# Kernel tuning notes

Hardware: AMD Instinct MI355X
Metric: run time of the kernel (lower is better)

## Reference

```python
import jax, jax.numpy as jnp
import numpy as np

D_MODEL = 1024
NUM_HEADS = 16
D_K = D_MODEL // NUM_HEADS


def setup_inputs() -> dict:
    key = jax.random.key(0)
    ks = jax.random.split(key, 9)
    s = 1.0 / np.sqrt(D_MODEL)
    return {
        "z": jax.random.normal(ks[0], (4, 2048, D_MODEL), dtype=jnp.float32),
        "Wq": jax.random.uniform(ks[1], (D_MODEL, D_MODEL), jnp.float32, -s, s),
        "bq": jax.random.uniform(ks[2], (D_MODEL,), jnp.float32, -s, s),
        "Wk": jax.random.uniform(ks[3], (D_MODEL, D_MODEL), jnp.float32, -s, s),
        "bk": jax.random.uniform(ks[4], (D_MODEL,), jnp.float32, -s, s),
        "Wv": jax.random.uniform(ks[5], (D_MODEL, D_MODEL), jnp.float32, -s, s),
        "bv": jax.random.uniform(ks[6], (D_MODEL,), jnp.float32, -s, s),
        "Wo": jax.random.uniform(ks[7], (D_MODEL, D_MODEL), jnp.float32, -s, s),
        "bo": jax.random.uniform(ks[8], (D_MODEL,), jnp.float32, -s, s),
    }


def reference(z, Wq, bq, Wk, bk, Wv, bv, Wo, bo):
    B, S, _ = z.shape
    # project and split heads: [B, H, S, d_k]
    def proj(W, b):
        return (z @ W.T + b).reshape(B, S, NUM_HEADS, D_K).transpose(0, 2, 1, 3)
    Q, K, V = proj(Wq, bq), proj(Wk, bk), proj(Wv, bv)
    scale = 1.0 / np.sqrt(D_K)
    scores = jnp.einsum('bhqd,bhkd->bhqk', Q, K) * scale
    probs = jax.nn.softmax(scores, axis=-1)
    ctx = jnp.einsum('bhqk,bhkd->bhqd', probs, V)
    ctx = ctx.transpose(0, 2, 1, 3).reshape(B, S, D_MODEL)
    return ctx @ Wo.T + bo
```

## Files before the change

### kernel.cpp

```cpp
#include <hip/hip_runtime.h>
#include <stdint.h>

#define D_MODEL 1024
#define NHEAD 16
#define DKH 64
#define BATCH 4
#define SEQ 2048
#define M_ROWS (BATCH*SEQ)
#define NBH (BATCH*NHEAD)

typedef float f32x4 __attribute__((ext_vector_type(4)));
typedef float f32x16 __attribute__((ext_vector_type(16)));
typedef __bf16 bf16x8 __attribute__((ext_vector_type(8)));
typedef __bf16 bf16x4v __attribute__((ext_vector_type(4)));
typedef short short4v __attribute__((ext_vector_type(4)));
typedef unsigned short ushort4v __attribute__((ext_vector_type(4)));
typedef unsigned short ushort8v __attribute__((ext_vector_type(8)));
typedef unsigned int uint2v __attribute__((ext_vector_type(2)));

__device__ __forceinline__ unsigned short f2bf(float x) {
    __bf16 b = (__bf16)x;
    return __builtin_bit_cast(unsigned short, b);
}

#define GLL(gsrc, ldst) \
    __builtin_amdgcn_global_load_lds((const __attribute__((address_space(1))) void*)(gsrc), \
                                     (__attribute__((address_space(3))) void*)(ldst), 16, 0, 0)


__device__ __forceinline__ void cvt8store(const float* __restrict__ src,
                                          unsigned short* __restrict__ dst) {
    float4 v0 = *(const float4*)(src);
    float4 v1 = *(const float4*)(src + 4);
    ushort8v o;
    o[0] = f2bf(v0.x); o[1] = f2bf(v0.y); o[2] = f2bf(v0.z); o[3] = f2bf(v0.w);
    o[4] = f2bf(v1.x); o[5] = f2bf(v1.y); o[6] = f2bf(v1.z); o[7] = f2bf(v1.w);
    *(ushort8v*)dst = o;
}

__global__ __launch_bounds__(256) void k_convert(
    const float* __restrict__ z,  const float* __restrict__ wq,
    const float* __restrict__ wk, const float* __restrict__ wv,
    const float* __restrict__ wo,
    const float* __restrict__ bq, const float* __restrict__ bk,
    const float* __restrict__ bv,
    unsigned short* __restrict__ zf, unsigned short* __restrict__ wqkvf,
    unsigned short* __restrict__ wobf, float* __restrict__ biasf)
{
    int i = blockIdx.x * 256 + threadIdx.x;
    if (i < 1048576) {
        int lane = i & 63, rest = i >> 6;
        int kk = rest & 1, mfrag = (rest >> 1) & 7, half = (rest >> 4) & 1;
        int kt = (rest >> 5) & 15, mtile = rest >> 9;
        int row = mtile * 256 + half * 128 + mfrag * 16 + (lane & 15);
        int k = kt * 64 + kk * 32 + (lane >> 4) * 8;
        cvt8store(z + (size_t)row * 1024 + k, zf + (size_t)i * 8);
    }
    int i2 = i - 1048576;
    if (i2 >= 0 && i2 < 393216) {
        int lane = i2 & 63, rest = i2 >> 6;
        int kk = rest & 1, nfrag = (rest >> 1) & 7;
        int kt = (rest >> 4) & 15, ntile = rest >> 8;
        int n = ntile * 128 + nfrag * 16 + (lane & 15);
        int k = kt * 64 + kk * 32 + (lane >> 4) * 8;
        const float* W = (n < 1024) ? wq : ((n < 2048) ? wk : wv);
        cvt8store(W + (size_t)(n & 1023) * 1024 + k, wqkvf + (size_t)i2 * 8);
    }
    int i3 = i2 - 393216;
    if (i3 >= 0 && i3 < 131072) {
        int lane = i3 & 63, rest = i3 >> 6;
        int kk = rest & 1, nfrag = (rest >> 1) & 7;
        int kt = (rest >> 4) & 15, ntile = rest >> 8;
        int n = ntile * 128 + nfrag * 16 + (lane & 15);
        int k = kt * 64 + kk * 32 + (lane >> 4) * 8;
        cvt8store(wo + (size_t)n * 1024 + k, wobf + (size_t)i3 * 8);
    }
    if (i < 1024) {
        biasf[i]        = bq[i];
        biasf[1024 + i] = bk[i];
        biasf[2048 + i] = bv[i];
    }
}

__device__ __forceinline__ void g_stage(const unsigned short* __restrict__ as_,
                                        const unsigned short* __restrict__ bs_,
                                        unsigned short* la, unsigned short* lb,
                                        int wid, int lane)
{
#pragma unroll
    for (int g = 0; g < 4; ++g)
        GLL(as_ + (wid + 8 * g) * 512 + lane * 8, la + (wid + 8 * g) * 512);
#pragma unroll
    for (int g = 0; g < 2; ++g)
        GLL(bs_ + (wid + 8 * g) * 512 + lane * 8, lb + (wid + 8 * g) * 512);
}

#define GEMM_KLOOP(Abase, Bbase)                                                      \
    g_stage(Abase, Bbase, &ldsA[0][0], &ldsB[0][0], wid, lane);                       \
    g_stage(Abase + 16384, Bbase + 8192, &ldsA[1][0], &ldsB[1][0], wid, lane);        \
    asm volatile("s_waitcnt vmcnt(6)" ::: "memory");                                  \
    __builtin_amdgcn_s_barrier();                                                     \
    for (int t = 0; t < 16; ++t) {                                                    \
        int buf = t % 3;                                                              \
        if (t + 2 < 16)                                                               \
            g_stage(Abase + (size_t)(t + 2) * 16384, Bbase + (size_t)(t + 2) * 8192,  \
                    &ldsA[(t + 2) % 3][0], &ldsB[(t + 2) % 3][0], wid, lane);         \
        const unsigned short* A = &ldsA[buf][0];                                      \
        const unsigned short* B = &ldsB[buf][0];                                      \
        bf16x8 b00 = *(const bf16x8*)(B + ((wn * 2 + 0) * 2 + 0) * 512 + lane * 8);   \
        bf16x8 b01 = *(const bf16x8*)(B + ((wn * 2 + 0) * 2 + 1) * 512 + lane * 8);   \
        bf16x8 b10 = *(const bf16x8*)(B + ((wn * 2 + 1) * 2 + 0) * 512 + lane * 8);   \
        bf16x8 b11 = *(const bf16x8*)(B + ((wn * 2 + 1) * 2 + 1) * 512 + lane * 8);   \
        _Pragma("unroll")                                                             \
        for (int ii = 0; ii < 8; ++ii) {                                              \
            bf16x8 a0 = *(const bf16x8*)(A + ((wm * 8 + ii) * 2 + 0) * 512 + lane * 8); \
            bf16x8 a1 = *(const bf16x8*)(A + ((wm * 8 + ii) * 2 + 1) * 512 + lane * 8); \
            acc[ii][0] = __builtin_amdgcn_mfma_f32_16x16x32_bf16(a0, b00, acc[ii][0], 0, 0, 0); \
            acc[ii][0] = __builtin_amdgcn_mfma_f32_16x16x32_bf16(a1, b01, acc[ii][0], 0, 0, 0); \
            acc[ii][1] = __builtin_amdgcn_mfma_f32_16x16x32_bf16(a0, b10, acc[ii][1], 0, 0, 0); \
            acc[ii][1] = __builtin_amdgcn_mfma_f32_16x16x32_bf16(a1, b11, acc[ii][1], 0, 0, 0); \
        }                                                                             \
        if (t < 14)       { asm volatile("s_waitcnt vmcnt(6)" ::: "memory"); }        \
        else if (t == 14) { asm volatile("s_waitcnt vmcnt(0)" ::: "memory"); }        \
        if (t < 15) { __builtin_amdgcn_sched_barrier(0); __builtin_amdgcn_s_barrier(); } \
    }

__global__ __launch_bounds__(512) void k_gemm_qkv(
    const unsigned short* __restrict__ Af,
    const unsigned short* __restrict__ Bf,
    const float* __restrict__ biasf,
    unsigned short* __restrict__ qb, unsigned short* __restrict__ kfrag,
    unsigned short* __restrict__ vfrag)
{
    __shared__ unsigned short ldsA[3][16384];
    __shared__ unsigned short ldsB[3][8192];

    int bid = blockIdx.x;
    int wg = (bid & 7) * 96 + (bid >> 3);
    int tn = wg % 24, tm = wg / 24;
    int tid = threadIdx.x, wid = tid >> 6, lane = tid & 63;
    int wm = wid >> 2, wn = wid & 3;

    const unsigned short* Abase = Af + (size_t)tm * 16 * 16384;
    const unsigned short* Bbase = Bf + (size_t)tn * 16 * 8192;

    f32x4 acc[8][2] = {};
    GEMM_KLOOP(Abase, Bbase)

    const float QSC = 0.18033688011112042f;
    int t3 = tn >> 3;
#pragma unroll
    for (int j = 0; j < 2; ++j) {
        int col = tn * 128 + wn * 32 + j * 16 + (lane & 15);
        float bias = biasf[col];
        int d = col & 1023, h = d >> 6, dk = d & 63;
#pragma unroll
        for (int i = 0; i < 8; ++i) {
#pragma unroll
            for (int r = 0; r < 4; ++r) {
                int row = tm * 256 + wm * 128 + i * 16 + (lane >> 4) * 4 + r;
                float v = acc[i][j][r] + bias;
                if (t3 == 0) v *= QSC;
                unsigned short bv16 = f2bf(v);
                int b_ = row >> 11, s_ = row & 2047;
                int bh = b_ * NHEAD + h;
                if (t3 == 0) {
                    qb[((size_t)bh * SEQ + s_) * DKH + dk] = bv16;
                } else if (t3 == 1) {
                    int kvblk = s_ >> 6, r64 = s_ & 63;
                    int t32 = r64 >> 5, l5 = r64 & 31;
                    int ds = dk >> 4, hi2 = (dk >> 3) & 1, e = dk & 7;
                    kfrag[((size_t)(bh * 32 + kvblk)) * 4096 +
                          (t32 * 4 + ds) * 512 + (hi2 * 32 + l5) * 8 + e] = bv16;
                } else {
                    int kvblk = s_ >> 6, kv64 = s_ & 63;
                    int ks = kv64 >> 3, hi2 = (kv64 >> 2) & 1, e = kv64 & 3;
                    int vt = dk >> 5, l5 = dk & 31;
                    vfrag[((size_t)(bh * 32 + kvblk)) * 4096 +
                          (vt * 8 + ks) * 256 + (hi2 * 32 + l5) * 4 + e] = bv16;
                }
            }
        }
    }
}

#define ATTN_STEP(LDSK, LDSV, WPREV, WCUR, DO_PV)                                   \
    {                                                                               \
        f32x16 st0 = {}, st1 = {};                                                  \
        __builtin_amdgcn_s_setprio(1);                                              \
        _Pragma("unroll")                                                           \
        for (int ds = 0; ds < 4; ++ds) {                                            \
            bf16x8 kf0 = *(const bf16x8*)(&(LDSK)[(ds) * 512 + lane * 8]);          \
            bf16x8 kf1 = *(const bf16x8*)(&(LDSK)[(4 + ds) * 512 + lane * 8]);      \
            st0 = __builtin_amdgcn_mfma_f32_32x32x16_bf16(kf0, aq[ds], st0, 0, 0, 0); \
            st1 = __builtin_amdgcn_mfma_f32_32x32x16_bf16(kf1, aq[ds], st1, 0, 0, 0); \
            if (DO_PV) {                                                            \
                short4v vf0 = *(const short4v*)(&(LDSV)[(2 * ds) * 256 + lane * 4]);        \
                short4v vf1 = *(const short4v*)(&(LDSV)[(8 + 2 * ds) * 256 + lane * 4]);    \
                oa0 = __builtin_amdgcn_mfma_f32_32x32x8bf16_1k(vf0, WPREV[2 * ds], oa0, 0, 0, 0); \
                oa1 = __builtin_amdgcn_mfma_f32_32x32x8bf16_1k(vf1, WPREV[2 * ds], oa1, 0, 0, 0); \
                short4v vf2 = *(const short4v*)(&(LDSV)[(2 * ds + 1) * 256 + lane * 4]);    \
                short4v vf3 = *(const short4v*)(&(LDSV)[(8 + 2 * ds + 1) * 256 + lane * 4]);\
                oa0 = __builtin_amdgcn_mfma_f32_32x32x8bf16_1k(vf2, WPREV[2 * ds + 1], oa0, 0, 0, 0); \
                oa1 = __builtin_amdgcn_mfma_f32_32x32x8bf16_1k(vf3, WPREV[2 * ds + 1], oa1, 0, 0, 0); \
            }                                                                       \
        }                                                                           \
        __builtin_amdgcn_s_setprio(0);                                              \
        _Pragma("unroll")                                                           \
        for (int ks = 0; ks < 4; ++ks) {                                            \
            {                                                                       \
                float p0 = __builtin_amdgcn_exp2f(st0[4 * ks + 0]);                 \
                float p1 = __builtin_amdgcn_exp2f(st0[4 * ks + 1]);                 \
                float p2 = __builtin_amdgcn_exp2f(st0[4 * ks + 2]);                 \
                float p3 = __builtin_amdgcn_exp2f(st0[4 * ks + 3]);                 \
                lsum += (p0 + p1) + (p2 + p3);                                      \
                bf16x4v pb;                                                         \
                pb[0] = (__bf16)p0; pb[1] = (__bf16)p1; pb[2] = (__bf16)p2; pb[3] = (__bf16)p3; \
                WCUR[ks] = __builtin_bit_cast(short4v, pb);                         \
            }                                                                       \
            {                                                                       \
                float p0 = __builtin_amdgcn_exp2f(st1[4 * ks + 0]);                 \
                float p1 = __builtin_amdgcn_exp2f(st1[4 * ks + 1]);                 \
                float p2 = __builtin_amdgcn_exp2f(st1[4 * ks + 2]);                 \
                float p3 = __builtin_amdgcn_exp2f(st1[4 * ks + 3]);                 \
                lsum += (p0 + p1) + (p2 + p3);                                      \
                bf16x4v pb;                                                         \
                pb[0] = (__bf16)p0; pb[1] = (__bf16)p1; pb[2] = (__bf16)p2; pb[3] = (__bf16)p3; \
                WCUR[4 + ks] = __builtin_bit_cast(short4v, pb);                     \
            }                                                                       \
        }                                                                           \
    }

#define DRAIN_BARRIER()                                         \
    asm volatile("s_waitcnt vmcnt(0)" ::: "memory");            \
    __builtin_amdgcn_sched_barrier(0);                          \
    __builtin_amdgcn_s_barrier();

__global__ __launch_bounds__(512) void k_attn(
    const unsigned short* __restrict__ qg,
    const unsigned short* __restrict__ kb,
    const unsigned short* __restrict__ vtb,
    unsigned short* __restrict__ ctxf)
{
    __shared__ unsigned short lds_k[2][4096];
    __shared__ unsigned short lds_v[2][4096];

    int bid = blockIdx.x;
    int x = bid & 7, li = bid >> 3;
    int bh = x * 8 + (li >> 3);
    int qt = li & 7;

    int tid = threadIdx.x, wid = tid >> 6, lane = tid & 63;
    int lq = lane & 31, hi = lane >> 5;

    bf16x8 aq[4];
    {
        const unsigned short* qp = qg + ((size_t)bh * SEQ + qt * 256 + wid * 32 + lq) * DKH + hi * 8;
#pragma unroll
        for (int d = 0; d < 4; ++d) aq[d] = *(const bf16x8*)(qp + d * 16);
    }

    float lsum = 0.f;
    f32x16 oa0 = {};
    f32x16 oa1 = {};
    short4v wA[8], wB[8];

    const unsigned short* kbase = kb  + (size_t)bh * 32 * 4096;
    const unsigned short* vbase = vtb + (size_t)bh * 32 * 4096;
    int so = wid * 512 + lane * 8;
    unsigned short* ldk0 = &lds_k[0][wid * 512];
    unsigned short* ldk1 = &lds_k[1][wid * 512];
    unsigned short* ldv0 = &lds_v[0][wid * 512];
    unsigned short* ldv1 = &lds_v[1][wid * 512];

    GLL(kbase + so, ldk0);
    DRAIN_BARRIER();

    GLL(kbase + 4096 + so, ldk1);
    GLL(vbase + so, ldv0);
    ATTN_STEP(lds_k[0], lds_v[0], wB, wA, false);
    DRAIN_BARRIER();

    for (int t = 1; t < 31; t += 2) {
        GLL(kbase + (size_t)(t + 1) * 4096 + so, ldk0);
        GLL(vbase + (size_t)t * 4096 + so, ldv1);
        ATTN_STEP(lds_k[1], lds_v[0], wA, wB, true);
        DRAIN_BARRIER();
        if (t + 2 < 32) GLL(kbase + (size_t)(t + 2) * 4096 + so, ldk1);
        GLL(vbase + (size_t)(t + 1) * 4096 + so, ldv0);
        ATTN_STEP(lds_k[0], lds_v[1], wB, wA, true);
        DRAIN_BARRIER();
    }

    GLL(vbase + (size_t)31 * 4096 + so, ldv1);
    ATTN_STEP(lds_k[1], lds_v[0], wA, wB, true);
    DRAIN_BARRIER();

    __builtin_amdgcn_s_setprio(1);
#pragma unroll
    for (int ks = 0; ks < 8; ++ks) {
        short4v vf0 = *(const short4v*)(&lds_v[1][(ks) * 256 + lane * 4]);
        short4v vf1 = *(const short4v*)(&lds_v[1][(8 + ks) * 256 + lane * 4]);
        oa0 = __builtin_amdgcn_mfma_f32_32x32x8bf16_1k(vf0, wB[ks], oa0, 0, 0, 0);
        oa1 = __builtin_amdgcn_mfma_f32_32x32x8bf16_1k(vf1, wB[ks], oa1, 0, 0, 0);
    }
    __builtin_amdgcn_s_setprio(0);

    int b_ = bh >> 4, h = bh & 15;
    lsum += __shfl_xor(lsum, 32);
    float inv = 1.0f / lsum;
    int s_ = qt * 256 + wid * 32 + lq;
    int row = b_ * 2048 + s_;
    int mtile = row >> 8, half = (row >> 7) & 1, mfrag = (row >> 4) & 7, lrow = row & 15;
    unsigned short* cb = ctxf + (size_t)((mtile * 16 + h) * 2 + half) * 8192
                              + mfrag * 1024 + lrow * 8 + 4 * hi;
#pragma unroll
    for (int m = 0; m < 4; ++m) {
        ushort4v s0, s1;
        s0[0] = f2bf(oa0[4 * m + 0] * inv); s0[1] = f2bf(oa0[4 * m + 1] * inv);
        s0[2] = f2bf(oa0[4 * m + 2] * inv); s0[3] = f2bf(oa0[4 * m + 3] * inv);
        *(ushort4v*)(cb + m * 128) = s0;
        s1[0] = f2bf(oa1[4 * m + 0] * inv); s1[1] = f2bf(oa1[4 * m + 1] * inv);
        s1[2] = f2bf(oa1[4 * m + 2] * inv); s1[3] = f2bf(oa1[4 * m + 3] * inv);
        *(ushort4v*)(cb + 512 + m * 128) = s1;
    }
}

__global__ __launch_bounds__(512) void k_gemm_out(
    const unsigned short* __restrict__ Af,
    const unsigned short* __restrict__ Bf,
    const float* __restrict__ bo,
    float* __restrict__ out)
{
    __shared__ unsigned short ldsA[3][16384];
    __shared__ unsigned short ldsB[3][8192];

    int bid = blockIdx.x;
    int wg = (bid & 7) * 32 + (bid >> 3);
    int tn = wg % 8, tm = wg / 8;
    int tid = threadIdx.x, wid = tid >> 6, lane = tid & 63;
    int wm = wid >> 2, wn = wid & 3;

    const unsigned short* Abase = Af + (size_t)tm * 16 * 16384;
    const unsigned short* Bbase = Bf + (size_t)tn * 16 * 8192;

    f32x4 acc[8][2] = {};
    GEMM_KLOOP(Abase, Bbase)

#pragma unroll
    for (int j = 0; j < 2; ++j) {
        int col = tn * 128 + wn * 32 + j * 16 + (lane & 15);
        float bias = bo[col];
#pragma unroll
        for (int i = 0; i < 8; ++i) {
#pragma unroll
            for (int r = 0; r < 4; ++r) {
                int row = tm * 256 + wm * 128 + i * 16 + (lane >> 4) * 4 + r;
                out[(size_t)row * 1024 + col] = acc[i][j][r] + bias;
            }
        }
    }
}

extern "C" void kernel_launch(void* const* d_in, const int* in_sizes, int n_in,
                              void* d_out, int out_size, void* d_ws, size_t ws_size,
                              hipStream_t stream)
{
    const float* z  = (const float*)d_in[0];
    const float* Wq = (const float*)d_in[1];
    const float* bq = (const float*)d_in[2];
    const float* Wk = (const float*)d_in[3];
    const float* bk = (const float*)d_in[4];
    const float* Wv = (const float*)d_in[5];
    const float* bv = (const float*)d_in[6];
    const float* Wo = (const float*)d_in[7];
    const float* bo = (const float*)d_in[8];
    float* out = (float*)d_out;

    char* ws = (char*)d_ws;
    unsigned short* zf    = (unsigned short*)(ws);
    unsigned short* ctxf  = (unsigned short*)(ws);
    unsigned short* wqkvf = (unsigned short*)(ws + (16ull << 20));
    unsigned short* wobf  = (unsigned short*)(ws + (22ull << 20));
    float*          biasf = (float*)(ws + (24ull << 20));
    unsigned short* qb    = (unsigned short*)(ws + (25ull << 20));
    unsigned short* kfrag = (unsigned short*)(ws + (41ull << 20));
    unsigned short* vfrag = (unsigned short*)(ws + (57ull << 20));

    k_convert<<<8192, 256, 0, stream>>>(z, Wq, Wk, Wv, Wo, bq, bk, bv, zf, wqkvf, wobf, biasf);
    k_gemm_qkv<<<768, 512, 0, stream>>>(zf, wqkvf, biasf, qb, kfrag, vfrag);
    k_attn<<<NBH * 8, 512, 0, stream>>>(qb, kfrag, vfrag, ctxf);
    k_gemm_out<<<256, 512, 0, stream>>>(ctxf, wobf, bo, out);
}
```

Before: 214.2 us.

## Use 32x32x16 bf16 MFMA for PV with permlane32 swap for P fragments

Switches the P·V product from the older 32x32x8 MFMA to the 32x32x16 instruction, halving the PV MFMA count. The V fragment layout written by the projection kernel is changed to match, and V is read from LDS in 8-element vectors. Softmax probabilities are packed as bf16 pairs and redistributed across lane halves with permlane32_swap to form the wider B operand. This adds cross-lane permutes per step and depends on the new V layout being consistent with the MFMA operand mapping.

Result: no change. 214.6 us (+0.1%).

```diff
diff --git a/kernel.cpp b/kernel.cpp
--- a/kernel.cpp
+++ b/kernel.cpp
@@ -12,15 +12,18 @@
 typedef float f32x4 __attribute__((ext_vector_type(4)));
 typedef float f32x16 __attribute__((ext_vector_type(16)));
 typedef __bf16 bf16x8 __attribute__((ext_vector_type(8)));
-typedef __bf16 bf16x4v __attribute__((ext_vector_type(4)));
 typedef short short4v __attribute__((ext_vector_type(4)));
 typedef unsigned short ushort4v __attribute__((ext_vector_type(4)));
 typedef unsigned short ushort8v __attribute__((ext_vector_type(8)));
-typedef unsigned int uint2v __attribute__((ext_vector_type(2)));
+typedef int int2v __attribute__((ext_vector_type(2)));
+typedef int int4v __attribute__((ext_vector_type(4)));
 
 __device__ __forceinline__ unsigned short f2bf(float x) {
     __bf16 b = (__bf16)x;
     return __builtin_bit_cast(unsigned short, b);
+}
+__device__ __forceinline__ unsigned int packbf2(float lo, float hi) {
+    return (unsigned int)f2bf(lo) | ((unsigned int)f2bf(hi) << 16);
 }
 
 #define GLL(gsrc, ldst) \
@@ -174,10 +177,10 @@
                           (t32 * 4 + ds) * 512 + (hi2 * 32 + l5) * 8 + e] = bv16;
                 } else {
                     int kvblk = s_ >> 6, kv64 = s_ & 63;
-                    int ks = kv64 >> 3, hi2 = (kv64 >> 2) & 1, e = kv64 & 3;
+                    int s16 = kv64 >> 4, hi2 = (kv64 >> 3) & 1, e = kv64 & 7;
                     int vt = dk >> 5, l5 = dk & 31;
                     vfrag[((size_t)(bh * 32 + kvblk)) * 4096 +
-                          (vt * 8 + ks) * 256 + (hi2 * 32 + l5) * 4 + e] = bv16;
+                          (vt * 4 + s16) * 512 + (hi2 * 32 + l5) * 8 + e] = bv16;
                 }
             }
         }
@@ -195,39 +198,35 @@
             st0 = __builtin_amdgcn_mfma_f32_32x32x16_bf16(kf0, aq[ds], st0, 0, 0, 0); \
             st1 = __builtin_amdgcn_mfma_f32_32x32x16_bf16(kf1, aq[ds], st1, 0, 0, 0); \
             if (DO_PV) {                                                            \
-                short4v vf0 = *(const short4v*)(&(LDSV)[(2 * ds) * 256 + lane * 4]);        \
-                short4v vf1 = *(const short4v*)(&(LDSV)[(8 + 2 * ds) * 256 + lane * 4]);    \
-                oa0 = __builtin_amdgcn_mfma_f32_32x32x8bf16_1k(vf0, WPREV[2 * ds], oa0, 0, 0, 0); \
-                oa1 = __builtin_amdgcn_mfma_f32_32x32x8bf16_1k(vf1, WPREV[2 * ds], oa1, 0, 0, 0); \
-                short4v vf2 = *(const short4v*)(&(LDSV)[(2 * ds + 1) * 256 + lane * 4]);    \
-                short4v vf3 = *(const short4v*)(&(LDSV)[(8 + 2 * ds + 1) * 256 + lane * 4]);\
-                oa0 = __builtin_amdgcn_mfma_f32_32x32x8bf16_1k(vf2, WPREV[2 * ds + 1], oa0, 0, 0, 0); \
-                oa1 = __builtin_amdgcn_mfma_f32_32x32x8bf16_1k(vf3, WPREV[2 * ds + 1], oa1, 0, 0, 0); \
+                bf16x8 vf0 = *(const bf16x8*)(&(LDSV)[(ds) * 512 + lane * 8]);      \
+                bf16x8 vf1 = *(const bf16x8*)(&(LDSV)[(4 + ds) * 512 + lane * 8]);  \
+                oa0 = __builtin_amdgcn_mfma_f32_32x32x16_bf16(vf0, WPREV[ds], oa0, 0, 0, 0); \
+                oa1 = __builtin_amdgcn_mfma_f32_32x32x16_bf16(vf1, WPREV[ds], oa1, 0, 0, 0); \
             }                                                                       \
         }                                                                           \
         __builtin_amdgcn_s_setprio(0);                                              \
+        unsigned int w16[16];                                                       \
         _Pragma("unroll")                                                           \
-        for (int ks = 0; ks < 4; ++ks) {                                            \
-            {                                                                       \
-                float p0 = __builtin_amdgcn_exp2f(st0[4 * ks + 0]);                 \
-                float p1 = __builtin_amdgcn_exp2f(st0[4 * ks + 1]);                 \
-                float p2 = __builtin_amdgcn_exp2f(st0[4 * ks + 2]);                 \
-                float p3 = __builtin_amdgcn_exp2f(st0[4 * ks + 3]);                 \
-                lsum += (p0 + p1) + (p2 + p3);                                      \
-                bf16x4v pb;                                                         \
-                pb[0] = (__bf16)p0; pb[1] = (__bf16)p1; pb[2] = (__bf16)p2; pb[3] = (__bf16)p3; \
-                WCUR[ks] = __builtin_bit_cast(short4v, pb);                         \
-            }                                                                       \
-            {                                                                       \
-                float p0 = __builtin_amdgcn_exp2f(st1[4 * ks + 0]);                 \
-                float p1 = __builtin_amdgcn_exp2f(st1[4 * ks + 1]);                 \
-                float p2 = __builtin_amdgcn_exp2f(st1[4 * ks + 2]);                 \
-                float p3 = __builtin_amdgcn_exp2f(st1[4 * ks + 3]);                 \
-                lsum += (p0 + p1) + (p2 + p3);                                      \
-                bf16x4v pb;                                                         \
-                pb[0] = (__bf16)p0; pb[1] = (__bf16)p1; pb[2] = (__bf16)p2; pb[3] = (__bf16)p3; \
-                WCUR[4 + ks] = __builtin_bit_cast(short4v, pb);                     \
-            }                                                                       \
+        for (int jj = 0; jj < 8; ++jj) {                                            \
+            float p0 = __builtin_amdgcn_exp2f(st0[2 * jj]);                         \
+            float p1 = __builtin_amdgcn_exp2f(st0[2 * jj + 1]);                     \
+            lsum += p0 + p1;                                                        \
+            w16[jj] = packbf2(p0, p1);                                              \
+        }                                                                           \
+        _Pragma("unroll")                                                           \
+        for (int jj = 0; jj < 8; ++jj) {                                            \
+            float p0 = __builtin_amdgcn_exp2f(st1[2 * jj]);                         \
+            float p1 = __builtin_amdgcn_exp2f(st1[2 * jj + 1]);                     \
+            lsum += p0 + p1;                                                        \
+            w16[8 + jj] = packbf2(p0, p1);                                          \
+        }                                                                           \
+        _Pragma("unroll")                                                           \
+        for (int s = 0; s < 4; ++s) {                                               \
+            int base = (s >> 1) * 8 + (s & 1) * 4;                                  \
+            int2v r1 = __builtin_amdgcn_permlane32_swap((int)w16[base + 0], (int)w16[base + 2], false, false); \
+            int2v r2 = __builtin_amdgcn_permlane32_swap((int)w16[base + 1], (int)w16[base + 3], false, false); \
+            int4v fr; fr[0] = r1[0]; fr[1] = r2[0]; fr[2] = r1[1]; fr[3] = r2[1];   \
+            WCUR[s] = __builtin_bit_cast(bf16x8, fr);                               \
         }                                                                           \
     }
 
@@ -263,7 +262,7 @@
     float lsum = 0.f;
     f32x16 oa0 = {};
     f32x16 oa1 = {};
-    short4v wA[8], wB[8];
+    bf16x8 wA[4], wB[4];
 
     const unsigned short* kbase = kb  + (size_t)bh * 32 * 4096;
     const unsigned short* vbase = vtb + (size_t)bh * 32 * 4096;
@@ -298,11 +297,11 @@
 
     __builtin_amdgcn_s_setprio(1);
 #pragma unroll
-    for (int ks = 0; ks < 8; ++ks) {
-        short4v vf0 = *(const short4v*)(&lds_v[1][(ks) * 256 + lane * 4]);
-        short4v vf1 = *(const short4v*)(&lds_v[1][(8 + ks) * 256 + lane * 4]);
-        oa0 = __builtin_amdgcn_mfma_f32_32x32x8bf16_1k(vf0, wB[ks], oa0, 0, 0, 0);
-        oa1 = __builtin_amdgcn_mfma_f32_32x32x8bf16_1k(vf1, wB[ks], oa1, 0, 0, 0);
+    for (int s = 0; s < 4; ++s) {
+        bf16x8 vf0 = *(const bf16x8*)(&lds_v[1][(s) * 512 + lane * 8]);
+        bf16x8 vf1 = *(const bf16x8*)(&lds_v[1][(4 + s) * 512 + lane * 8]);
+        oa0 = __builtin_amdgcn_mfma_f32_32x32x16_bf16(vf0, wB[s], oa0, 0, 0, 0);
+        oa1 = __builtin_amdgcn_mfma_f32_32x32x16_bf16(vf1, wB[s], oa1, 0, 0, 0);
     }
     __builtin_amdgcn_s_setprio(0);
 
```
